# Kernel optimization log

Hardware: AMD Instinct MI355X
Metric: run time of the kernel (lower is better)

The kernel has to match this reference:

```python
import jax, jax.numpy as jnp
import numpy as np

B = 256           # puzzles per batch
C = 128           # hidden_channels
L = 8             # num_layers
H, D = 4, 32      # heads, out per head (H*D == C, concat=True)
N_CELLS = 81
EPS_LN = 1e-5
NEG_SLOPE = 0.2   # PyG GATv2Conv default


def _sudoku_edges():
    # replicates GNNModel._create_sudoku_edges: row0=src, row1=dst, 1620 edges
    edges = []
    for r in range(9):
        for c in range(9):
            src = r * 9 + c
            nb = set()
            for k in range(9):
                if k != c:
                    nb.add(r * 9 + k)
                if k != r:
                    nb.add(k * 9 + c)
            br, bc = r // 3, c // 3
            for i in range(br * 3, br * 3 + 3):
                for j in range(bc * 3, bc * 3 + 3):
                    if i != r or j != c:
                        nb.add(i * 9 + j)
            for d in sorted(nb):
                edges.append((src, d))
    return np.array(edges, dtype=np.int32).T  # [2, 1620]


def setup_inputs() -> dict:
    key = jax.random.key(0)
    ks = jax.random.split(key, 8)
    base = _sudoku_edges()                                   # [2, 1620]
    shift = np.arange(B, dtype=np.int32) * N_CELLS
    ei = (base[:, None, :] + shift[None, :, None]).reshape(2, -1)  # [2, B*1620]
    s = 1.0 / np.sqrt(C)
    return {
        "x": jax.random.randint(ks[0], (B, 9, 9), 0, 10, dtype=jnp.int32),
        "edge_index": jnp.asarray(ei),
        "embed_w": jax.random.normal(ks[1], (10, C), jnp.float32) * 0.1,
        "Wl": jax.random.normal(ks[2], (L, C, C), jnp.float32) * s,
        "bl": jnp.zeros((L, C), jnp.float32),
        "Wr": jax.random.normal(ks[3], (L, C, C), jnp.float32) * s,
        "br": jnp.zeros((L, C), jnp.float32),
        "att": jax.random.normal(ks[4], (L, H, D), jnp.float32) * 0.1,
        "conv_b": jnp.zeros((L, C), jnp.float32),
        "ln_w": jnp.ones((L, C), jnp.float32),
        "ln_b": jnp.zeros((L, C), jnp.float32),
        "cls_w": jax.random.normal(ks[5], (C, 9), jnp.float32) * s,
        "cls_b": jnp.zeros((9,), jnp.float32),
    }


def _segment_softmax(logits, seg, n):
    # numerically stable per-destination-node softmax (PyG softmax semantics)
    m = jax.ops.segment_max(logits, seg, num_segments=n)
    e = jnp.exp(logits - m[seg])
    s = jax.ops.segment_sum(e, seg, num_segments=n)
    return e / (s[seg] + 1e-16)


def reference(x, edge_index, embed_w, Wl, bl, Wr, br, att, conv_b,
              ln_w, ln_b, cls_w, cls_b):
    N = B * N_CELLS
    h = embed_w[x.reshape(-1)]                               # [N, C]
    src, dst = edge_index[0], edge_index[1]
    for l in range(L):  # fixed small layer count
        h_in = h
        xl = (h @ Wl[l] + bl[l]).reshape(N, H, D)            # lin_l(x) -> values/src
        xr = (h @ Wr[l] + br[l]).reshape(N, H, D)            # lin_r(x) -> dst
        e = jax.nn.leaky_relu(xl[src] + xr[dst], NEG_SLOPE)  # [E, H, D]
        logits = jnp.einsum('ehd,hd->eh', e, att[l])         # [E, H]
        alpha = _segment_softmax(logits, dst, N)             # [E, H]
        out = jax.ops.segment_sum(xl[src] * alpha[..., None], dst,
                                  num_segments=N)            # [N, H, D]
        out = out.reshape(N, C) + conv_b[l]
        # PyG LayerNorm(mode='graph') with batch=None: global mean/std
        g = out - out.mean()
        g = g / (g.std() + EPS_LN)
        h = jax.nn.relu(g * ln_w[l] + ln_b[l]) + h_in        # dropout off (eval)
    logits = h @ cls_w + cls_b                               # [N, 9]
    return logits.reshape(B, 9, 9, 9)
```

## Files before the change

### kernel.cpp

```cpp
#include <hip/hip_runtime.h>
#include <string.h>

#define NPZ 81
#define NNODES 20736
#define CH 128
#define NHEAD 4
#define NB 20
#define NLAY 8
#define TPB 512

typedef __attribute__((ext_vector_type(4))) float f32x4;
typedef __attribute__((ext_vector_type(8))) __bf16 bf16x8;
typedef __attribute__((ext_vector_type(8))) unsigned short u16x8;

#define SW(n, hh, c4) ((c4) ^ (((n) & 7) ^ ((hh) << 1)))

__device__ __forceinline__ unsigned short f2bf(float f) {
  unsigned int u = __float_as_uint(f);
  u = (u + 0x7fffu + ((u >> 16) & 1u)) >> 16;
  return (unsigned short)u;
}

struct alignas(16) Slot { float s1, s2; unsigned int flag; unsigned int pad; };

__launch_bounds__(TPB, 1)
__global__ void k_fused(const int* __restrict__ x, const float* __restrict__ ew,
                        const float* __restrict__ Wl, const float* __restrict__ bl,
                        const float* __restrict__ Wr, const float* __restrict__ br,
                        const float* __restrict__ att, const float* __restrict__ convb,
                        const float* __restrict__ lnw, const float* __restrict__ lnb,
                        const float* __restrict__ clsw, const float* __restrict__ clsb,
                        u16x8* __restrict__ wpk, Slot* __restrict__ slots,
                        float* __restrict__ logits) {
  __shared__ float h_f[NPZ * 128];
  __shared__ unsigned short h_s[NPZ * 136];
  __shared__ float xl_s[NPZ * 128];
  __shared__ float xr_s[NPZ * 128];
  __shared__ int nb_s[NPZ * NB];
  __shared__ float att_s[CH], cvb_s[CH], bias_s[256], lnw_s[CH], lnb_s[CH];
  __shared__ float red_s[18];

  const int tid = threadIdx.x;
  const int pz = blockIdx.x;
  const int n0 = pz * NPZ;

  if (tid < NPZ) {
    const int r = tid / 9, cq = tid % 9;
    int c2 = tid * NB;
    for (int k = 0; k < 9; ++k) if (k != cq) nb_s[c2++] = r * 9 + k;
    for (int k = 0; k < 9; ++k) if (k != r) nb_s[c2++] = k * 9 + cq;
    const int br0 = (r / 3) * 3, bc0 = (cq / 3) * 3;
    for (int i = br0; i < br0 + 3; ++i)
      for (int jj = bc0; jj < bc0 + 3; ++jj)
        if (i != r && jj != cq) nb_s[c2++] = i * 9 + jj;
  }

  for (int m = tid; m < NPZ * 32; m += TPB) {
    const int j = m >> 5, c4 = m & 31;
    const int xv = x[n0 + j];
    const f32x4 v = ((const f32x4*)ew)[xv * 32 + c4];
    *(f32x4*)&h_f[j * 128 + c4 * 4] = v;
    const unsigned int lo = (unsigned int)f2bf(v[0]) | ((unsigned int)f2bf(v[1]) << 16);
    const unsigned int hi = (unsigned int)f2bf(v[2]) | ((unsigned int)f2bf(v[3]) << 16);
    *(uint2*)&h_s[j * 136 + c4 * 4] = make_uint2(lo, hi);
  }

  if (tid < 128) {
    const int t = pz * 128 + tid;
    const int lane = t & 63;
    const int kb = (t >> 6) & 3;
    const int nt = (t >> 8) & 15;
    const int l = t >> 12;
    const int cc = nt * 16 + (lane & 15);
    const int k0 = kb * 32 + (lane >> 4) * 8;
    const float* W = (cc < CH) ? (Wl + (size_t)l * CH * CH + cc)
                               : (Wr + (size_t)l * CH * CH + (cc - CH));
    u16x8 v;
#pragma unroll
    for (int e = 0; e < 8; ++e) v[e] = f2bf(W[(size_t)(k0 + e) * CH]);
    unsigned long long w0, w1;
    memcpy(&w0, &v, 8);
    memcpy(&w1, ((const char*)&v) + 8, 8);
    unsigned long long* dst = (unsigned long long*)&wpk[t];
    __hip_atomic_store(&dst[0], w0, __ATOMIC_RELAXED, __HIP_MEMORY_SCOPE_AGENT);
    __hip_atomic_store(&dst[1], w1, __ATOMIC_RELAXED, __HIP_MEMORY_SCOPE_AGENT);
  }

  __syncthreads();
  if (tid == 0)
    __hip_atomic_store(&slots[8 * 256 + pz].flag, 1u, __ATOMIC_RELAXED, __HIP_MEMORY_SCOPE_AGENT);
  if (tid < 64) {
    bool done = false;
    while (!done) {
      bool ok = true;
#pragma unroll
      for (int q = 0; q < 4; ++q)
        ok &= (__hip_atomic_load(&slots[8 * 256 + tid + q * 64].flag, __ATOMIC_RELAXED,
                                 __HIP_MEMORY_SCOPE_AGENT) == 1u);
      done = __all(ok);
      if (!done) __builtin_amdgcn_s_sleep(1);
    }
  }
  __syncthreads();

  const int wv = tid >> 6, lane = tid & 63;
  const int l15 = lane & 15, l4 = lane >> 4;

#pragma unroll 1
  for (int l = 0; l < NLAY; ++l) {
    bf16x8 bfr[2][4];
#pragma unroll
    for (int ni = 0; ni < 2; ++ni)
#pragma unroll
      for (int kb = 0; kb < 4; ++kb)
        bfr[ni][kb] = ((const bf16x8*)wpk)[(((size_t)l * 16 + (wv * 2 + ni)) * 4 + kb) * 64 + lane];

    if (tid < 256) bias_s[tid] = (tid < CH) ? bl[l * CH + tid] : br[l * CH + tid - CH];
    else if (tid < 384) att_s[tid - 256] = att[l * CH + (tid - 256)] * 0.6f;
    else cvb_s[tid - 384] = convb[l * CH + (tid - 384)];
    if (tid < 128) lnw_s[tid] = lnw[l * CH + tid];
    else if (tid < 256) lnb_s[tid - 128] = lnb[l * CH + tid - 128];
    __syncthreads();

    {
#pragma unroll
      for (int mt = 0; mt < 6; ++mt) {
        int arow = mt * 16 + l15; arow = arow > 80 ? 80 : arow;
        bf16x8 afr[4];
#pragma unroll
        for (int kb = 0; kb < 4; ++kb)
          afr[kb] = *(const bf16x8*)&h_s[arow * 136 + kb * 32 + l4 * 8];
#pragma unroll
        for (int ni = 0; ni < 2; ++ni) {
          f32x4 acc = {0.f, 0.f, 0.f, 0.f};
#pragma unroll
          for (int kb = 0; kb < 4; ++kb)
            acc = __builtin_amdgcn_mfma_f32_16x16x32_bf16(afr[kb], bfr[ni][kb], acc, 0, 0, 0);
          const int cc = (wv * 2 + ni) * 16 + l15;
          const float bia = bias_s[cc];
          float* dst = (cc < CH) ? xl_s : xr_s;
          const int c127 = cc & 127;
          const int hh = c127 >> 5;
          const int c4 = (c127 >> 2) & 7, el = c127 & 3;
#pragma unroll
          for (int i = 0; i < 4; ++i) {
            const int row = mt * 16 + l4 * 4 + i;
            if (row < NPZ)
              dst[row * 128 + hh * 32 + SW(row, hh, c4) * 4 + el] = acc[i] + bia;
          }
        }
      }
    }
    __syncthreads();

    float psum = 0.f, psumsq = 0.f;
    f32x4 o[8];
    const int j = tid >> 2, hh = tid & 3;
    if (tid < NPZ * NHEAD) {
      f32x4 xr4[8], ar[8];
#pragma unroll
      for (int c4 = 0; c4 < 8; ++c4) {
        xr4[c4] = *(const f32x4*)&xr_s[j * 128 + hh * 32 + SW(j, hh, c4) * 4];
        ar[c4] = *(const f32x4*)&att_s[hh * 32 + c4 * 4];
      }
      float m = -3.0e38f, ssum = 0.f;
      f32x4 oacc[8] = {};
      for (int k = 0; k < NB; k += 2) {
        const int nb1 = nb_s[j * NB + k];
        const int nb2 = nb_s[j * NB + k + 1];
        f32x4 v1[8], v2[8];
#pragma unroll
        for (int c4 = 0; c4 < 8; ++c4) {
          v1[c4] = *(const f32x4*)&xl_s[nb1 * 128 + hh * 32 + SW(nb1, hh, c4) * 4];
          v2[c4] = *(const f32x4*)&xl_s[nb2 * 128 + hh * 32 + SW(nb2, hh, c4) * 4];
        }
        float a0 = 0.f, a1 = 0.f, a2 = 0.f, a3 = 0.f;
        float b0 = 0.f, b1 = 0.f, b2 = 0.f, b3 = 0.f;
#pragma unroll
        for (int c4 = 0; c4 < 8; ++c4) {
          const f32x4 sA = v1[c4] + xr4[c4];
          const f32x4 sB = v2[c4] + xr4[c4];
          f32x4 uA, uB;
#pragma unroll
          for (int q = 0; q < 4; ++q) {
            uA[q] = fmaf(0.66666667f, fabsf(sA[q]), sA[q]);
            uB[q] = fmaf(0.66666667f, fabsf(sB[q]), sB[q]);
          }
          a0 = fmaf(uA[0], ar[c4][0], a0); b0 = fmaf(uB[0], ar[c4][0], b0);
          a1 = fmaf(uA[1], ar[c4][1], a1); b1 = fmaf(uB[1], ar[c4][1], b1);
          a2 = fmaf(uA[2], ar[c4][2], a2); b2 = fmaf(uB[2], ar[c4][2], b2);
          a3 = fmaf(uA[3], ar[c4][3], a3); b3 = fmaf(uB[3], ar[c4][3], b3);
        }
        const float lgA = (a0 + a1) + (a2 + a3);
        const float lgB = (b0 + b1) + (b2 + b3);
        const float nm = fmaxf(m, fmaxf(lgA, lgB));
        const float sc = __expf(m - nm);
        const float eA = __expf(lgA - nm);
        const float eB = __expf(lgB - nm);
        ssum = fmaf(ssum, sc, eA + eB);
#pragma unroll
        for (int c4 = 0; c4 < 8; ++c4) {
          f32x4 t = oacc[c4] * sc;
          t = v1[c4] * eA + t;
          t = v2[c4] * eB + t;
          oacc[c4] = t;
        }
        m = nm;
      }
      const float rs = 1.f / ssum;
#pragma unroll
      for (int c4 = 0; c4 < 8; ++c4) {
        o[c4] = oacc[c4] * rs + *(const f32x4*)&cvb_s[hh * 32 + c4 * 4];
        psum += (o[c4][0] + o[c4][1]) + (o[c4][2] + o[c4][3]);
        psumsq += (o[c4][0] * o[c4][0] + o[c4][1] * o[c4][1]) +
                  (o[c4][2] * o[c4][2] + o[c4][3] * o[c4][3]);
      }
    }

#pragma unroll
    for (int mm = 1; mm < 64; mm <<= 1) {
      psum += __shfl_xor(psum, mm, 64);
      psumsq += __shfl_xor(psumsq, mm, 64);
    }
    if ((tid & 63) == 0) { red_s[wv * 2] = psum; red_s[wv * 2 + 1] = psumsq; }
    __syncthreads();

    if (tid >= 448) {
      const int pl = tid - 448;
      if (tid == 511) {
        float a = 0.f, b = 0.f;
#pragma unroll
        for (int i = 0; i < 8; ++i) { a += red_s[i * 2]; b += red_s[i * 2 + 1]; }
        Slot* sl = &slots[l * 256 + pz];
        const float2 f2 = make_float2(a, b);
        unsigned long long uv;
        memcpy(&uv, &f2, 8);
        __hip_atomic_store((unsigned long long*)&sl->s1, uv, __ATOMIC_RELAXED, __HIP_MEMORY_SCOPE_AGENT);
        asm volatile("s_waitcnt vmcnt(0)" ::: "memory");
        __hip_atomic_store(&sl->flag, 1u, __ATOMIC_RELAXED, __HIP_MEMORY_SCOPE_AGENT);
      }
      bool done = false;
      while (!done) {
        bool ok = true;
#pragma unroll
        for (int q = 0; q < 4; ++q)
          ok &= (__hip_atomic_load(&slots[l * 256 + pl + q * 64].flag, __ATOMIC_RELAXED,
                                   __HIP_MEMORY_SCOPE_AGENT) == 1u);
        done = __all(ok);
        if (!done) __builtin_amdgcn_s_sleep(1);
      }
      float s1 = 0.f, s2 = 0.f;
#pragma unroll
      for (int q = 0; q < 4; ++q) {
        const unsigned long long uv = __hip_atomic_load(
            (unsigned long long*)&slots[l * 256 + pl + q * 64].s1, __ATOMIC_RELAXED,
            __HIP_MEMORY_SCOPE_AGENT);
        float2 f2;
        memcpy(&f2, &uv, 8);
        s1 += f2.x; s2 += f2.y;
      }
#pragma unroll
      for (int mm = 1; mm < 64; mm <<= 1) {
        s1 += __shfl_xor(s1, mm, 64);
        s2 += __shfl_xor(s2, mm, 64);
      }
      if (tid == 448) {
        const float M = (float)NNODES * CH;
        const float mean = s1 / M;
        const float var = fmaxf(s2 / M - mean * mean, 0.f);
        red_s[16] = mean;
        red_s[17] = 1.f / (sqrtf(var) + 1e-5f);
      }
    } else if (tid < NPZ * NHEAD) {
#pragma unroll
      for (int c4 = 0; c4 < 8; ++c4)
        *(f32x4*)&xl_s[j * 128 + hh * 32 + SW(j, hh, c4) * 4] = o[c4];
    }
    __syncthreads();
    const float mean = red_s[16], inv = red_s[17];

    for (int m = tid; m < NPZ * 32; m += TPB) {
      const int jj = m >> 5, c4m = m & 31;
      const int hh2 = c4m >> 3, q = c4m & 7;
      const f32x4 ov = *(const f32x4*)&xl_s[jj * 128 + hh2 * 32 + SW(jj, hh2, q) * 4];
      f32x4 hv = *(f32x4*)&h_f[jj * 128 + c4m * 4];
#pragma unroll
      for (int e = 0; e < 4; ++e) {
        const float g = (ov[e] - mean) * inv;
        hv[e] += fmaxf(g * lnw_s[c4m * 4 + e] + lnb_s[c4m * 4 + e], 0.f);
      }
      *(f32x4*)&h_f[jj * 128 + c4m * 4] = hv;
      const unsigned int lo = (unsigned int)f2bf(hv[0]) | ((unsigned int)f2bf(hv[1]) << 16);
      const unsigned int hi = (unsigned int)f2bf(hv[2]) | ((unsigned int)f2bf(hv[3]) << 16);
      *(uint2*)&h_s[jj * 136 + c4m * 4] = make_uint2(lo, hi);
    }
    __syncthreads();
  }

  for (int idx = tid; idx < CH * 9; idx += TPB) {
    const int k = idx / 9, c = idx - k * 9;
    xr_s[k * 12 + c] = clsw[idx];
  }
  __syncthreads();
  for (int t2 = tid; t2 < NPZ * 9; t2 += TPB) {
    const int j2 = t2 / 9, c = t2 - j2 * 9;
    const int kc0 = tid & 31;
    float acc = clsb[c];
#pragma unroll 8
    for (int kc = 0; kc < 32; ++kc) {
      const int cc4 = (kc0 + kc) & 31;
      const f32x4 hv = *(const f32x4*)&h_f[j2 * 128 + cc4 * 4];
      acc += hv[0] * xr_s[(cc4 * 4 + 0) * 12 + c] + hv[1] * xr_s[(cc4 * 4 + 1) * 12 + c] +
             hv[2] * xr_s[(cc4 * 4 + 2) * 12 + c] + hv[3] * xr_s[(cc4 * 4 + 3) * 12 + c];
    }
    logits[(size_t)(n0 + j2) * 9 + c] = acc;
  }
}

extern "C" void kernel_launch(void* const* d_in, const int* in_sizes, int n_in,
                              void* d_out, int out_size, void* d_ws, size_t ws_size,
                              hipStream_t stream) {
  const int* x = (const int*)d_in[0];
  const float* ew = (const float*)d_in[2];
  const float* Wl = (const float*)d_in[3];
  const float* bl = (const float*)d_in[4];
  const float* Wr = (const float*)d_in[5];
  const float* br = (const float*)d_in[6];
  const float* att = (const float*)d_in[7];
  const float* cvb = (const float*)d_in[8];
  const float* lnw = (const float*)d_in[9];
  const float* lnb = (const float*)d_in[10];
  const float* clsw = (const float*)d_in[11];
  const float* clsb = (const float*)d_in[12];

  char* ws = (char*)d_ws;
  u16x8* wpk = (u16x8*)ws;
  Slot* slots = (Slot*)(ws + 524288);
  float* logits = (float*)d_out;

  (void)hipMemsetAsync(ws + 524288, 0, 9 * 256 * 16, stream);

  void* args[] = {(void*)&x, (void*)&ew, (void*)&Wl, (void*)&bl, (void*)&Wr, (void*)&br,
                  (void*)&att, (void*)&cvb, (void*)&lnw, (void*)&lnb, (void*)&clsw,
                  (void*)&clsb, (void*)&wpk, (void*)&slots, (void*)&logits};
  (void)hipLaunchCooperativeKernel((void*)k_fused, dim3(256), dim3(TPB), args, 0, stream);
}
```

Measured before the change: 191.1 us.

## Split leaky-relu attention into linear and abs terms; widen block to 768 threads

Rewrites leaky_relu(s)·a as 0.6·a·s + 0.4·a·|s|, so the linear part is precomputed per node (al_s for sources, arj for the destination) and only the |s| term is evaluated per edge. The block grows to 768 threads, with two threads per (node, head), each handling 16 channels and combining partial logits via a shuffle. The GEMM is remapped to one n-tile per wave over two passes, and the LayerNorm/residual update is applied straight from registers, dropping a staging write to shared memory. The gain is fewer per-edge FLOPs and more parallel threads, at the cost of extra shuffles, an added barrier and higher register pressure under the new launch bounds.

```diff
diff --git a/kernel.cpp b/kernel.cpp
--- a/kernel.cpp
+++ b/kernel.cpp
@@ -7,7 +7,7 @@
 #define NHEAD 4
 #define NB 20
 #define NLAY 8
-#define TPB 512
+#define TPB 768
 
 typedef __attribute__((ext_vector_type(4))) float f32x4;
 typedef __attribute__((ext_vector_type(8))) __bf16 bf16x8;
@@ -23,7 +23,7 @@
 
 struct alignas(16) Slot { float s1, s2; unsigned int flag; unsigned int pad; };
 
-__launch_bounds__(TPB, 1)
+__launch_bounds__(TPB, 3)
 __global__ void k_fused(const int* __restrict__ x, const float* __restrict__ ew,
                         const float* __restrict__ Wl, const float* __restrict__ bl,
                         const float* __restrict__ Wr, const float* __restrict__ br,
@@ -37,8 +37,9 @@
   __shared__ float xl_s[NPZ * 128];
   __shared__ float xr_s[NPZ * 128];
   __shared__ int nb_s[NPZ * NB];
-  __shared__ float att_s[CH], cvb_s[CH], bias_s[256], lnw_s[CH], lnb_s[CH];
-  __shared__ float red_s[18];
+  __shared__ float att6_s[CH], att4_s[CH], cvb_s[CH], bias_s[256], lnw_s[CH], lnb_s[CH];
+  __shared__ float al_s[NPZ * 4];
+  __shared__ float red_s[26];
 
   const int tid = threadIdx.x;
   const int pz = blockIdx.x;
@@ -105,24 +106,28 @@
 
   const int wv = tid >> 6, lane = tid & 63;
   const int l15 = lane & 15, l4 = lane >> 4;
+  const int p = tid >> 1, half = tid & 1;
+  const int j = p >> 2, hh = p & 3;
+  const int cbase = hh * 32 + half * 16;
 
 #pragma unroll 1
   for (int l = 0; l < NLAY; ++l) {
-    bf16x8 bfr[2][4];
-#pragma unroll
-    for (int ni = 0; ni < 2; ++ni)
+    if (tid < 256) bias_s[tid] = (tid < CH) ? bl[l * CH + tid] : br[l * CH + tid - CH];
+    else if (tid < 384) att6_s[tid - 256] = att[l * CH + (tid - 256)] * 0.6f;
+    else if (tid < 512) att4_s[tid - 384] = att[l * CH + (tid - 384)] * 0.4f;
+    else if (tid < 640) cvb_s[tid - 512] = convb[l * CH + (tid - 512)];
+    else lnw_s[tid - 640] = lnw[l * CH + (tid - 640)];
+    if (tid < 128) lnb_s[tid] = lnb[l * CH + tid];
+    __syncthreads();
+
+#pragma unroll 1
+    for (int pass = 0; pass < 2; ++pass) {
+      if (pass == 1 && wv >= 4) break;
+      const int nt = (pass == 0) ? wv : 12 + wv;
+      bf16x8 bfr[4];
 #pragma unroll
       for (int kb = 0; kb < 4; ++kb)
-        bfr[ni][kb] = ((const bf16x8*)wpk)[(((size_t)l * 16 + (wv * 2 + ni)) * 4 + kb) * 64 + lane];
-
-    if (tid < 256) bias_s[tid] = (tid < CH) ? bl[l * CH + tid] : br[l * CH + tid - CH];
-    else if (tid < 384) att_s[tid - 256] = att[l * CH + (tid - 256)] * 0.6f;
-    else cvb_s[tid - 384] = convb[l * CH + (tid - 384)];
-    if (tid < 128) lnw_s[tid] = lnw[l * CH + tid];
-    else if (tid < 256) lnb_s[tid - 128] = lnb[l * CH + tid - 128];
-    __syncthreads();
-
-    {
+        bfr[kb] = ((const bf16x8*)wpk)[(((size_t)l * 16 + nt) * 4 + kb) * 64 + lane];
 #pragma unroll
       for (int mt = 0; mt < 6; ++mt) {
         int arow = mt * 16 + l15; arow = arow > 80 ? 80 : arow;
@@ -130,90 +135,93 @@
 #pragma unroll
         for (int kb = 0; kb < 4; ++kb)
           afr[kb] = *(const bf16x8*)&h_s[arow * 136 + kb * 32 + l4 * 8];
-#pragma unroll
-        for (int ni = 0; ni < 2; ++ni) {
-          f32x4 acc = {0.f, 0.f, 0.f, 0.f};
-#pragma unroll
-          for (int kb = 0; kb < 4; ++kb)
-            acc = __builtin_amdgcn_mfma_f32_16x16x32_bf16(afr[kb], bfr[ni][kb], acc, 0, 0, 0);
-          const int cc = (wv * 2 + ni) * 16 + l15;
-          const float bia = bias_s[cc];
-          float* dst = (cc < CH) ? xl_s : xr_s;
-          const int c127 = cc & 127;
-          const int hh = c127 >> 5;
-          const int c4 = (c127 >> 2) & 7, el = c127 & 3;
-#pragma unroll
-          for (int i = 0; i < 4; ++i) {
-            const int row = mt * 16 + l4 * 4 + i;
-            if (row < NPZ)
-              dst[row * 128 + hh * 32 + SW(row, hh, c4) * 4 + el] = acc[i] + bia;
+        f32x4 acc = {0.f, 0.f, 0.f, 0.f};
+#pragma unroll
+        for (int kb = 0; kb < 4; ++kb)
+          acc = __builtin_amdgcn_mfma_f32_16x16x32_bf16(afr[kb], bfr[kb], acc, 0, 0, 0);
+        const int cc = nt * 16 + l15;
+        const float bia = bias_s[cc];
+        float* dst = (cc < CH) ? xl_s : xr_s;
+        const int c127 = cc & 127;
+        const int dh = c127 >> 5;
+        const int c4 = (c127 >> 2) & 7, el = c127 & 3;
+#pragma unroll
+        for (int i = 0; i < 4; ++i) {
+          const int row = mt * 16 + l4 * 4 + i;
+          if (row < NPZ)
+            dst[row * 128 + dh * 32 + SW(row, dh, c4) * 4 + el] = acc[i] + bia;
+        }
+      }
+    }
+    __syncthreads();
+
+    f32x4 xr4[4], ar[4], o[4];
+    float arj = 0.f;
+    if (tid < NPZ * NHEAD * 2) {
+      float alp = 0.f, arp = 0.f;
+#pragma unroll
+      for (int q = 0; q < 4; ++q) {
+        const int c4 = half * 4 + q;
+        xr4[q] = *(const f32x4*)&xr_s[j * 128 + hh * 32 + SW(j, hh, c4) * 4];
+        ar[q] = *(const f32x4*)&att4_s[cbase + q * 4];
+        const f32x4 xv = *(const f32x4*)&xl_s[j * 128 + hh * 32 + SW(j, hh, c4) * 4];
+        const f32x4 a6 = *(const f32x4*)&att6_s[cbase + q * 4];
+#pragma unroll
+        for (int e = 0; e < 4; ++e) {
+          alp = fmaf(a6[e], xv[e], alp);
+          arp = fmaf(a6[e], xr4[q][e], arp);
+        }
+      }
+      alp += __shfl_xor(alp, 1, 64);
+      arj = arp + __shfl_xor(arp, 1, 64);
+      if (half == 0) al_s[j * 4 + hh] = alp;
+    }
+    __syncthreads();
+
+    float psum = 0.f, psumsq = 0.f;
+    if (tid < NPZ * NHEAD * 2) {
+      float m = -3.0e38f, ssum = 0.f;
+      f32x4 oacc[4] = {};
+      for (int k = 0; k < NB; k += 2) {
+        const int2 nbp = *(const int2*)&nb_s[j * NB + k];
+        const float al1 = al_s[nbp.x * 4 + hh];
+        const float al2 = al_s[nbp.y * 4 + hh];
+        f32x4 v1[4], v2[4];
+        float pa = 0.f, pb = 0.f;
+#pragma unroll
+        for (int q = 0; q < 4; ++q) {
+          const int c4 = half * 4 + q;
+          v1[q] = *(const f32x4*)&xl_s[nbp.x * 128 + hh * 32 + SW(nbp.x, hh, c4) * 4];
+          v2[q] = *(const f32x4*)&xl_s[nbp.y * 128 + hh * 32 + SW(nbp.y, hh, c4) * 4];
+#pragma unroll
+          for (int e = 0; e < 4; ++e) {
+            pa = fmaf(ar[q][e], fabsf(v1[q][e] + xr4[q][e]), pa);
+            pb = fmaf(ar[q][e], fabsf(v2[q][e] + xr4[q][e]), pb);
           }
         }
-      }
-    }
-    __syncthreads();
-
-    float psum = 0.f, psumsq = 0.f;
-    f32x4 o[8];
-    const int j = tid >> 2, hh = tid & 3;
-    if (tid < NPZ * NHEAD) {
-      f32x4 xr4[8], ar[8];
-#pragma unroll
-      for (int c4 = 0; c4 < 8; ++c4) {
-        xr4[c4] = *(const f32x4*)&xr_s[j * 128 + hh * 32 + SW(j, hh, c4) * 4];
-        ar[c4] = *(const f32x4*)&att_s[hh * 32 + c4 * 4];
-      }
-      float m = -3.0e38f, ssum = 0.f;
-      f32x4 oacc[8] = {};
-      for (int k = 0; k < NB; k += 2) {
-        const int nb1 = nb_s[j * NB + k];
-        const int nb2 = nb_s[j * NB + k + 1];
-        f32x4 v1[8], v2[8];
-#pragma unroll
-        for (int c4 = 0; c4 < 8; ++c4) {
-          v1[c4] = *(const f32x4*)&xl_s[nb1 * 128 + hh * 32 + SW(nb1, hh, c4) * 4];
-          v2[c4] = *(const f32x4*)&xl_s[nb2 * 128 + hh * 32 + SW(nb2, hh, c4) * 4];
-        }
-        float a0 = 0.f, a1 = 0.f, a2 = 0.f, a3 = 0.f;
-        float b0 = 0.f, b1 = 0.f, b2 = 0.f, b3 = 0.f;
-#pragma unroll
-        for (int c4 = 0; c4 < 8; ++c4) {
-          const f32x4 sA = v1[c4] + xr4[c4];
-          const f32x4 sB = v2[c4] + xr4[c4];
-          f32x4 uA, uB;
-#pragma unroll
-          for (int q = 0; q < 4; ++q) {
-            uA[q] = fmaf(0.66666667f, fabsf(sA[q]), sA[q]);
-            uB[q] = fmaf(0.66666667f, fabsf(sB[q]), sB[q]);
-          }
-          a0 = fmaf(uA[0], ar[c4][0], a0); b0 = fmaf(uB[0], ar[c4][0], b0);
-          a1 = fmaf(uA[1], ar[c4][1], a1); b1 = fmaf(uB[1], ar[c4][1], b1);
-          a2 = fmaf(uA[2], ar[c4][2], a2); b2 = fmaf(uB[2], ar[c4][2], b2);
-          a3 = fmaf(uA[3], ar[c4][3], a3); b3 = fmaf(uB[3], ar[c4][3], b3);
-        }
-        const float lgA = (a0 + a1) + (a2 + a3);
-        const float lgB = (b0 + b1) + (b2 + b3);
+        const float lgA = al1 + arj + (pa + __shfl_xor(pa, 1, 64));
+        const float lgB = al2 + arj + (pb + __shfl_xor(pb, 1, 64));
         const float nm = fmaxf(m, fmaxf(lgA, lgB));
         const float sc = __expf(m - nm);
         const float eA = __expf(lgA - nm);
         const float eB = __expf(lgB - nm);
         ssum = fmaf(ssum, sc, eA + eB);
 #pragma unroll
-        for (int c4 = 0; c4 < 8; ++c4) {
-          f32x4 t = oacc[c4] * sc;
-          t = v1[c4] * eA + t;
-          t = v2[c4] * eB + t;
-          oacc[c4] = t;
+        for (int q = 0; q < 4; ++q) {
+          f32x4 t = oacc[q] * sc;
+          t = v1[q] * eA + t;
+          t = v2[q] * eB + t;
+          oacc[q] = t;
         }
         m = nm;
       }
       const float rs = 1.f / ssum;
 #pragma unroll
-      for (int c4 = 0; c4 < 8; ++c4) {
-        o[c4] = oacc[c4] * rs + *(const f32x4*)&cvb_s[hh * 32 + c4 * 4];
-        psum += (o[c4][0] + o[c4][1]) + (o[c4][2] + o[c4][3]);
-        psumsq += (o[c4][0] * o[c4][0] + o[c4][1] * o[c4][1]) +
-                  (o[c4][2] * o[c4][2] + o[c4][3] * o[c4][3]);
+      for (int q = 0; q < 4; ++q) {
+        o[q] = oacc[q] * rs + *(const f32x4*)&cvb_s[cbase + q * 4];
+        psum += (o[q][0] + o[q][1]) + (o[q][2] + o[q][3]);
+        psumsq += (o[q][0] * o[q][0] + o[q][1] * o[q][1]) +
+                  (o[q][2] * o[q][2] + o[q][3] * o[q][3]);
       }
     }
 
@@ -225,12 +233,12 @@
     if ((tid & 63) == 0) { red_s[wv * 2] = psum; red_s[wv * 2 + 1] = psumsq; }
     __syncthreads();
 
-    if (tid >= 448) {
-      const int pl = tid - 448;
-      if (tid == 511) {
+    if (tid >= 704) {
+      const int pl = tid - 704;
+      if (tid == 704) {
         float a = 0.f, b = 0.f;
 #pragma unroll
-        for (int i = 0; i < 8; ++i) { a += red_s[i * 2]; b += red_s[i * 2 + 1]; }
+        for (int i = 0; i < 12; ++i) { a += red_s[i * 2]; b += red_s[i * 2 + 1]; }
         Slot* sl = &slots[l * 256 + pz];
         const float2 f2 = make_float2(a, b);
         unsigned long long uv;
@@ -264,35 +272,32 @@
         s1 += __shfl_xor(s1, mm, 64);
         s2 += __shfl_xor(s2, mm, 64);
       }
-      if (tid == 448) {
+      if (tid == 704) {
         const float M = (float)NNODES * CH;
         const float mean = s1 / M;
         const float var = fmaxf(s2 / M - mean * mean, 0.f);
-        red_s[16] = mean;
-        red_s[17] = 1.f / (sqrtf(var) + 1e-5f);
-      }
-    } else if (tid < NPZ * NHEAD) {
-#pragma unroll
-      for (int c4 = 0; c4 < 8; ++c4)
-        *(f32x4*)&xl_s[j * 128 + hh * 32 + SW(j, hh, c4) * 4] = o[c4];
-    }
-    __syncthreads();
-    const float mean = red_s[16], inv = red_s[17];
-
-    for (int m = tid; m < NPZ * 32; m += TPB) {
-      const int jj = m >> 5, c4m = m & 31;
-      const int hh2 = c4m >> 3, q = c4m & 7;
-      const f32x4 ov = *(const f32x4*)&xl_s[jj * 128 + hh2 * 32 + SW(jj, hh2, q) * 4];
-      f32x4 hv = *(f32x4*)&h_f[jj * 128 + c4m * 4];
-#pragma unroll
-      for (int e = 0; e < 4; ++e) {
-        const float g = (ov[e] - mean) * inv;
-        hv[e] += fmaxf(g * lnw_s[c4m * 4 + e] + lnb_s[c4m * 4 + e], 0.f);
-      }
-      *(f32x4*)&h_f[jj * 128 + c4m * 4] = hv;
-      const unsigned int lo = (unsigned int)f2bf(hv[0]) | ((unsigned int)f2bf(hv[1]) << 16);
-      const unsigned int hi = (unsigned int)f2bf(hv[2]) | ((unsigned int)f2bf(hv[3]) << 16);
-      *(uint2*)&h_s[jj * 136 + c4m * 4] = make_uint2(lo, hi);
+        red_s[24] = mean;
+        red_s[25] = 1.f / (sqrtf(var) + 1e-5f);
+      }
+    }
+    __syncthreads();
+    const float mean = red_s[24], inv = red_s[25];
+
+    if (tid < NPZ * NHEAD * 2) {
+#pragma unroll
+      for (int q = 0; q < 4; ++q) {
+        const int cb = cbase + q * 4;
+        f32x4 hv = *(f32x4*)&h_f[j * 128 + cb];
+#pragma unroll
+        for (int e = 0; e < 4; ++e) {
+          const float g = (o[q][e] - mean) * inv;
+          hv[e] += fmaxf(g * lnw_s[cb + e] + lnb_s[cb + e], 0.f);
+        }
+        *(f32x4*)&h_f[j * 128 + cb] = hv;
+        const unsigned int lo = (unsigned int)f2bf(hv[0]) | ((unsigned int)f2bf(hv[1]) << 16);
+        const unsigned int hi = (unsigned int)f2bf(hv[2]) | ((unsigned int)f2bf(hv[3]) << 16);
+        *(uint2*)&h_s[j * 136 + cb] = make_uint2(lo, hi);
+      }
     }
     __syncthreads();
   }
```

After: 169.8 us. 11.1% less time.
